# Performance work log

Hardware: AMD Instinct MI355X
Metric: run time of the kernel (lower is better)

The kernel has to match this reference:

```python
import jax, jax.numpy as jnp
import numpy as np

B, S, D_IN, D_OUT = 8, 2048, 1024, 1024


def setup_inputs() -> dict:
    key = jax.random.key(0)
    ks = jax.random.split(key, 9)
    sc = 1.0 / np.sqrt(D_IN)
    return {
        "in_k": jax.random.normal(ks[0], (B, S, D_IN), jnp.float32),
        "in_q": jax.random.normal(ks[1], (B, S, D_IN), jnp.float32),
        "in_v": jax.random.normal(ks[2], (B, S, D_IN), jnp.float32),
        "Wk": jax.random.normal(ks[3], (D_IN, D_OUT), jnp.float32) * sc,
        "bk": jax.random.normal(ks[4], (D_OUT,), jnp.float32) * sc,
        "Wq": jax.random.normal(ks[5], (D_IN, D_OUT), jnp.float32) * sc,
        "bq": jax.random.normal(ks[6], (D_OUT,), jnp.float32) * sc,
        "Wv": jax.random.normal(ks[7], (D_IN, D_OUT), jnp.float32) * sc,
        "bv": jax.random.normal(ks[8], (D_OUT,), jnp.float32) * sc,
    }


def reference(in_k, in_q, in_v, Wk, bk, Wq, bq, Wv, bv):
    k = in_k @ Wk + bk  # [B,S,D]
    q = in_q @ Wq + bq
    v = in_v @ Wv + bv
    scale = 1.0 / jnp.sqrt(jnp.asarray(D_OUT, q.dtype))
    scores = jnp.einsum("bqd,bkd->bqk", q, k) * scale  # [B,S,S]
    attn = jax.nn.softmax(scores, axis=-1)
    return jnp.einsum("bqk,bkd->bqd", attn, v)
```

## Files before the change

kernel.cpp:

```cpp
#include <hip/hip_runtime.h>
#include <hip/hip_bf16.h>
#include <stdint.h>

typedef __bf16 bf16x8 __attribute__((ext_vector_type(8)));
typedef float  f32x4  __attribute__((ext_vector_type(4)));
typedef uint16_t u16x8 __attribute__((ext_vector_type(8)));

__device__ __forceinline__ uint16_t f32_to_bf16(float f) {
    union { float f; uint32_t u; } v; v.f = f;
    uint32_t u = v.u;
    uint32_t r = (u + 0x7FFFu + ((u >> 16) & 1u)) >> 16;
    return (uint16_t)r;
}

__device__ __forceinline__ void gld16(const void* g, void* l) {
    __builtin_amdgcn_global_load_lds(
        (const __attribute__((address_space(1))) void*)g,
        (__attribute__((address_space(3))) void*)l,
        16, 0, 0);
}

#define MFMA16 __builtin_amdgcn_mfma_f32_16x16x32_bf16
#define SBAR   __builtin_amdgcn_s_barrier
#define SCHED0() __builtin_amdgcn_sched_barrier(0)
#define PRIO   __builtin_amdgcn_s_setprio
#define VMCNT4() asm volatile("s_waitcnt vmcnt(4)" ::: "memory")
#define VMCNT0() asm volatile("s_waitcnt vmcnt(0)" ::: "memory")

__global__ __launch_bounds__(256) void cast3_kernel(
    const float* __restrict__ i0, const float* __restrict__ i1,
    const float* __restrict__ i2, uint16_t* __restrict__ o0,
    uint16_t* __restrict__ o1, uint16_t* __restrict__ o2) {
    const float* in = (blockIdx.z == 0) ? i0 : (blockIdx.z == 1) ? i1 : i2;
    uint16_t* out = (blockIdx.z == 0) ? o0 : (blockIdx.z == 1) ? o1 : o2;
    size_t i = ((size_t)blockIdx.x * 256 + threadIdx.x) * 8;
    float4 a = *(const float4*)(in + i);
    float4 b = *(const float4*)(in + i + 4);
    u16x8 o;
    o[0] = f32_to_bf16(a.x); o[1] = f32_to_bf16(a.y);
    o[2] = f32_to_bf16(a.z); o[3] = f32_to_bf16(a.w);
    o[4] = f32_to_bf16(b.x); o[5] = f32_to_bf16(b.y);
    o[6] = f32_to_bf16(b.z); o[7] = f32_to_bf16(b.w);
    *(u16x8*)(out + i) = o;
}

__global__ __launch_bounds__(256) void wtrans_kernel(
    const float* __restrict__ W0, const float* __restrict__ W1,
    const float* __restrict__ W2, uint16_t* __restrict__ Wt0) {
    const float* W = (blockIdx.z == 0) ? W0 : (blockIdx.z == 1) ? W1 : W2;
    uint16_t* Wt = Wt0 + (size_t)blockIdx.z * 1024 * 1024;
    __shared__ float tile[64][65];
    const int n0 = blockIdx.x * 64, k0 = blockIdx.y * 64;
    const int tx = threadIdx.x & 63, ty0 = threadIdx.x >> 6;
#pragma unroll
    for (int r = 0; r < 16; ++r) {
        int ty = ty0 + r * 4;
        tile[ty][tx] = W[(size_t)(k0 + ty) * 1024 + n0 + tx];
    }
    __syncthreads();
#pragma unroll
    for (int r = 0; r < 16; ++r) {
        int ty = ty0 + r * 4;
        Wt[(size_t)(n0 + ty) * 1024 + k0 + tx] = f32_to_bf16(tile[tx][ty]);
    }
}

__device__ __forceinline__ void stageA64(const uint16_t* __restrict__ G, int ldg,
                                         int k0, int rowbase, uint16_t* ldsT, int tid) {
    const int l = tid >> 3;
    const int ch = tid & 7;
    const int c = ((ch ^ (l & 7)) << 3);
    gld16(G + (size_t)(rowbase + l) * ldg + k0 + c,
          ldsT + (size_t)(rowbase + l) * 64 + ch * 8);
}

__device__ __forceinline__ void stageB64(const uint16_t* __restrict__ G, int ldg,
                                         int k0, int h, int j, uint16_t* ldsT, int tid) {
    const int lloc = j * 64 + (tid >> 3);
    const int ch = tid & 7;
    const int grow = (lloc & 31) + ((lloc >> 5) << 6) + (h << 5);
    const int c = ((ch ^ (lloc & 7)) << 3);
    gld16(G + (size_t)grow * ldg + k0 + c,
          ldsT + (size_t)(h * 128 + lloc) * 64 + ch * 8);
}

__device__ __forceinline__ void gemm_core(const uint16_t* __restrict__ A, int lda,
                                          const uint16_t* __restrict__ B, int ldb,
                                          int K, f32x4 (&acc)[8][4]) {
    __shared__ __align__(16) uint16_t As[2][16384];
    __shared__ __align__(16) uint16_t Bs[2][16384];
    const int tid  = threadIdx.x;
    const int lane = tid & 63;
    const int wave = tid >> 6;
    const int wr = wave >> 2, wcn = wave & 3;
    const int mrow = lane & 15, q = lane >> 4;
    const int sx = mrow & 7;
    const int c0 = ((q ^ sx) << 3);
    const int c1 = (((4 + q) ^ sx) << 3);
    const int abase = (wr * 128 + mrow) * 64;
    const int bb    = (wcn * 32 + mrow) * 64;

    const int NT = K >> 6;
    stageA64(A, lda, 0, 0,   As[0], tid);
    stageA64(A, lda, 0, 128, As[0], tid);
    SCHED0();
    stageB64(B, ldb, 0, 0, 0, Bs[0], tid);
    stageB64(B, ldb, 0, 0, 1, Bs[0], tid);
    SCHED0();
    stageB64(B, ldb, 0, 1, 0, Bs[0], tid);
    stageB64(B, ldb, 0, 1, 1, Bs[0], tid);
    SCHED0();
    stageA64(A, lda, 0, 64,  As[0], tid);
    stageA64(A, lda, 0, 192, As[0], tid);
    SCHED0();

    bf16x8 af[4][2], bA[2][2], bB[2][2];
    for (int t = 0; t < NT; ++t) {
        const int cur = t & 1;
        const uint16_t* as = As[cur];
        const uint16_t* bs = Bs[cur];
        uint16_t* An = As[cur ^ 1];
        uint16_t* Bn = Bs[cur ^ 1];
        const int kn = (t + 1 < NT) ? ((t + 1) << 6) : 0;

        VMCNT4();
        SBAR(); SCHED0();
        stageA64(A, lda, kn, 0,   An, tid);
        stageA64(A, lda, kn, 128, An, tid);
#pragma unroll
        for (int m = 0; m < 4; ++m) {
            af[m][0] = *(const bf16x8*)&as[abase + m * 1024 + c0];
            af[m][1] = *(const bf16x8*)&as[abase + m * 1024 + c1];
        }
#pragma unroll
        for (int n = 0; n < 2; ++n) {
            bA[n][0] = *(const bf16x8*)&bs[bb + n * 1024 + c0];
            bA[n][1] = *(const bf16x8*)&bs[bb + n * 1024 + c1];
        }
        SBAR(); SCHED0();
        PRIO(1);
#pragma unroll
        for (int m = 0; m < 4; ++m)
#pragma unroll
            for (int n = 0; n < 2; ++n) {
                acc[m][n] = MFMA16(af[m][0], bA[n][0], acc[m][n], 0, 0, 0);
                acc[m][n] = MFMA16(af[m][1], bA[n][1], acc[m][n], 0, 0, 0);
            }
        PRIO(0);

        VMCNT4();
        SBAR(); SCHED0();
        stageB64(B, ldb, kn, 0, 0, Bn, tid);
        stageB64(B, ldb, kn, 0, 1, Bn, tid);
#pragma unroll
        for (int n = 0; n < 2; ++n) {
            bB[n][0] = *(const bf16x8*)&bs[bb + 8192 + n * 1024 + c0];
            bB[n][1] = *(const bf16x8*)&bs[bb + 8192 + n * 1024 + c1];
        }
        SBAR(); SCHED0();
        PRIO(1);
#pragma unroll
        for (int m = 0; m < 4; ++m)
#pragma unroll
            for (int n = 0; n < 2; ++n) {
                acc[m][n + 2] = MFMA16(af[m][0], bB[n][0], acc[m][n + 2], 0, 0, 0);
                acc[m][n + 2] = MFMA16(af[m][1], bB[n][1], acc[m][n + 2], 0, 0, 0);
            }
        PRIO(0);

        VMCNT4();
        SBAR(); SCHED0();
        stageB64(B, ldb, kn, 1, 0, Bn, tid);
        stageB64(B, ldb, kn, 1, 1, Bn, tid);
#pragma unroll
        for (int m = 0; m < 4; ++m) {
            af[m][0] = *(const bf16x8*)&as[abase + (m + 4) * 1024 + c0];
            af[m][1] = *(const bf16x8*)&as[abase + (m + 4) * 1024 + c1];
        }
        SBAR(); SCHED0();
        PRIO(1);
#pragma unroll
        for (int m = 0; m < 4; ++m)
#pragma unroll
            for (int n = 0; n < 2; ++n) {
                acc[m + 4][n] = MFMA16(af[m][0], bA[n][0], acc[m + 4][n], 0, 0, 0);
                acc[m + 4][n] = MFMA16(af[m][1], bA[n][1], acc[m + 4][n], 0, 0, 0);
            }
        PRIO(0);

        SBAR(); SCHED0();
        stageA64(A, lda, kn, 64,  An, tid);
        stageA64(A, lda, kn, 192, An, tid);
        SBAR(); SCHED0();
        PRIO(1);
#pragma unroll
        for (int m = 0; m < 4; ++m)
#pragma unroll
            for (int n = 0; n < 2; ++n) {
                acc[m + 4][n + 2] = MFMA16(af[m][0], bB[n][0], acc[m + 4][n + 2], 0, 0, 0);
                acc[m + 4][n + 2] = MFMA16(af[m][1], bB[n][1], acc[m + 4][n + 2], 0, 0, 0);
            }
        PRIO(0);
    }
    VMCNT0();
}

__global__ __launch_bounds__(512, 2) void proj256_kernel(
    const uint16_t* __restrict__ Ab, const uint16_t* __restrict__ Bb,
    uint16_t* __restrict__ Cb, uint16_t* __restrict__ Vt,
    const float* __restrict__ b0, const float* __restrict__ b1,
    const float* __restrict__ b2) {
    const int bid = blockIdx.x;
    const int lg = (bid & 7) * 96 + (bid >> 3);
    const int pidx = lg >> 8;
    const int t = lg & 255;
    const int band = t >> 4;
    const int Mt = band * 4 + (t & 3);
    const int Nt = (t >> 2) & 3;
    const int row0 = Mt * 256, col0 = Nt * 256;

    const uint16_t* A = Ab + (size_t)pidx * 16777216 + (size_t)row0 * 1024;
    const uint16_t* B = Bb + (size_t)pidx * 1048576 + (size_t)col0 * 1024;
    const float* bias = (pidx == 0) ? b0 : (pidx == 1) ? b1 : b2;

    f32x4 acc[8][4];
#pragma unroll
    for (int i = 0; i < 8; ++i)
#pragma unroll
        for (int j = 0; j < 4; ++j) acc[i][j] = 0.0f;

    gemm_core(A, 1024, B, 1024, 1024, acc);

    const int tid = threadIdx.x, lane = tid & 63, wave = tid >> 6;
    const int wr = wave >> 2, wcn = wave & 3;
    const int mrow = lane & 15, quad = lane >> 4;
    float bv_[4];
#pragma unroll
    for (int n = 0; n < 4; ++n) bv_[n] = bias[col0 + wcn * 64 + n * 16 + mrow];

    if (pidx < 2) {
        uint16_t* C = Cb + (size_t)pidx * 16777216;
#pragma unroll
        for (int m = 0; m < 8; ++m)
#pragma unroll
            for (int n = 0; n < 4; ++n)
#pragma unroll
                for (int r = 0; r < 4; ++r) {
                    int row = row0 + wr * 128 + m * 16 + quad * 4 + r;
                    int col = col0 + wcn * 64 + n * 16 + mrow;
                    C[(size_t)row * 1024 + col] = f32_to_bf16(acc[m][n][r] + bv_[n]);
                }
    } else {
#pragma unroll
        for (int m = 0; m < 8; ++m)
#pragma unroll
            for (int n = 0; n < 4; ++n)
#pragma unroll
                for (int r = 0; r < 4; ++r) {
                    int row = row0 + wr * 128 + m * 16 + quad * 4 + r;
                    int col = col0 + wcn * 64 + n * 16 + mrow;
                    Vt[((size_t)(row >> 11) * 1024 + col) * 2048 + (row & 2047)] =
                        f32_to_bf16(acc[m][n][r] + bv_[n]);
                }
    }
}

template <int EPI>
__global__ __launch_bounds__(512, 2) void att256_kernel(
    const uint16_t* __restrict__ Abase, int lda, long long sAz,
    const uint16_t* __restrict__ Bbase, int ldb, long long sBz,
    void* __restrict__ Cv, int ldc, long long sCz,
    int K, float alpha, float* __restrict__ sums, int NtN, int chunk) {
    const int bid = blockIdx.x;
    const int lg = (bid & 7) * chunk + (bid >> 3);
    const int z = lg / chunk;
    const int t = lg % chunk;
    const int r2 = t & (2 * NtN - 1);
    const int band = t / (2 * NtN);
    const int Mt = band * 2 + (r2 & 1);
    const int Nt = r2 >> 1;
    const int row0 = Mt * 256, col0 = Nt * 256;

    const uint16_t* A = Abase + (size_t)z * sAz + (size_t)row0 * lda;
    const uint16_t* B = Bbase + (size_t)z * sBz + (size_t)col0 * ldb;

    f32x4 acc[8][4];
#pragma unroll
    for (int i = 0; i < 8; ++i)
#pragma unroll
        for (int j = 0; j < 4; ++j) acc[i][j] = 0.0f;

    gemm_core(A, lda, B, ldb, K, acc);

    const int tid = threadIdx.x, lane = tid & 63, wave = tid >> 6;
    const int wr = wave >> 2, wcn = wave & 3;
    const int mrow = lane & 15, quad = lane >> 4;

    if (EPI == 1) {
        uint16_t* C = (uint16_t*)Cv + (size_t)z * sCz;
#pragma unroll
        for (int m = 0; m < 8; ++m)
#pragma unroll
            for (int r = 0; r < 4; ++r) {
                int row = row0 + wr * 128 + m * 16 + quad * 4 + r;
                float s = 0.0f;
#pragma unroll
                for (int n = 0; n < 4; ++n) {
                    int col = col0 + wcn * 64 + n * 16 + mrow;
                    float e = __expf(acc[m][n][r] * alpha);
                    C[(size_t)row * ldc + col] = f32_to_bf16(e);
                    s += e;
                }
                s += __shfl_xor(s, 1, 64);
                s += __shfl_xor(s, 2, 64);
                s += __shfl_xor(s, 4, 64);
                s += __shfl_xor(s, 8, 64);
                if (mrow == 0) atomicAdd(&sums[(size_t)z * 2048 + row], s);
            }
    } else {
        float* C = (float*)Cv + (size_t)z * sCz;
#pragma unroll
        for (int m = 0; m < 8; ++m)
#pragma unroll
            for (int r = 0; r < 4; ++r) {
                int row = row0 + wr * 128 + m * 16 + quad * 4 + r;
                float inv = 1.0f / sums[(size_t)z * 2048 + row];
#pragma unroll
                for (int n = 0; n < 4; ++n) {
                    int col = col0 + wcn * 64 + n * 16 + mrow;
                    C[(size_t)row * ldc + col] = acc[m][n][r] * inv;
                }
            }
    }
}

extern "C" void kernel_launch(void* const* d_in, const int* in_sizes, int n_in,
                              void* d_out, int out_size, void* d_ws, size_t ws_size,
                              hipStream_t stream) {
    const float* in_k = (const float*)d_in[0];
    const float* in_q = (const float*)d_in[1];
    const float* in_v = (const float*)d_in[2];
    const float* Wk = (const float*)d_in[3];
    const float* bk = (const float*)d_in[4];
    const float* Wq = (const float*)d_in[5];
    const float* bq = (const float*)d_in[6];
    const float* Wv = (const float*)d_in[7];
    const float* bv = (const float*)d_in[8];
    float* out = (float*)d_out;

    char* w = (char*)d_ws;
    uint16_t* Xq  = (uint16_t*)(w + 0);
    uint16_t* Xk  = (uint16_t*)(w + 33554432);
    uint16_t* Xv  = (uint16_t*)(w + 67108864);
    uint16_t* Qb  = (uint16_t*)(w + 100663296);
    uint16_t* Kb  = (uint16_t*)(w + 134217728);
    uint16_t* Vt  = (uint16_t*)(w + 167772160);
    uint16_t* Wqt = (uint16_t*)(w + 201326592);
    uint16_t* Sc  = Xq;
    float*    sums = (float*)Xv;

    wtrans_kernel<<<dim3(16, 16, 3), 256, 0, stream>>>(Wq, Wk, Wv, Wqt);
    cast3_kernel<<<dim3(8192, 1, 3), 256, 0, stream>>>(in_q, in_k, in_v, Xq, Xk, Xv);

    proj256_kernel<<<768, 512, 0, stream>>>(Xq, Wqt, Qb, Vt, bq, bk, bv);

    hipMemsetAsync(sums, 0, 8 * 2048 * sizeof(float), stream);

    att256_kernel<1><<<512, 512, 0, stream>>>(
        Qb, 1024, 2048LL * 1024, Kb, 1024, 2048LL * 1024,
        Sc, 2048, 2048LL * 2048, 1024, 0.03125f, sums, 8, 64);

    att256_kernel<2><<<256, 512, 0, stream>>>(
        Sc, 2048, 2048LL * 2048, Vt, 2048, 1024LL * 2048,
        out, 1024, 2048LL * 1024, 2048, 1.0f, sums, 4, 32);
}
```

Before: 517.6 us.

## Software-pipeline LDS fragment reads one phase ahead of MFMA in projection GEMM

Restructures the projection GEMM main loop into a two-iteration unrolled 8-phase schedule. Each phase's LDS fragment reads for the next MFMA block are issued before the current MFMA block, using ping-pong register sets (Xa/Ya, Xb/Yb). Partial lgkmcnt and vmcnt waits let loads overlap compute instead of stalling on each read. This adds register pressure from the duplicated fragments and KEEP asm hacks to keep the dead prefetches alive. It also assumes NT is even and that the finer-grained waits are correct.

Measured after the change: 609.2 us. 1.18x slower.

```diff
diff --git a/kernel.cpp b/kernel.cpp
--- a/kernel.cpp
+++ b/kernel.cpp
@@ -24,8 +24,11 @@
 #define SBAR   __builtin_amdgcn_s_barrier
 #define SCHED0() __builtin_amdgcn_sched_barrier(0)
 #define PRIO   __builtin_amdgcn_s_setprio
-#define VMCNT4() asm volatile("s_waitcnt vmcnt(4)" ::: "memory")
+#define VMC2()   asm volatile("s_waitcnt vmcnt(2)" ::: "memory")
 #define VMCNT0() asm volatile("s_waitcnt vmcnt(0)" ::: "memory")
+#define LGKM4()  asm volatile("s_waitcnt lgkmcnt(4)" ::: "memory")
+#define LGKM8()  asm volatile("s_waitcnt lgkmcnt(8)" ::: "memory")
+#define KEEP(x)  asm volatile("" :: "v"(*(const float*)&(x)))
 
 __global__ __launch_bounds__(256) void cast3_kernel(
     const float* __restrict__ i0, const float* __restrict__ i1,
@@ -84,6 +87,37 @@
           ldsT + (size_t)(h * 128 + lloc) * 64 + ch * 8);
 }
 
+__device__ __forceinline__ void rdA(bf16x8 (&dst)[4][2], const uint16_t* s,
+                                    int abase, int mb, int c0, int c1) {
+#pragma unroll
+    for (int m = 0; m < 4; ++m) {
+        dst[m][0] = *(const bf16x8*)&s[abase + (mb + m) * 1024 + c0];
+        dst[m][1] = *(const bf16x8*)&s[abase + (mb + m) * 1024 + c1];
+    }
+}
+
+__device__ __forceinline__ void rdB(bf16x8 (&dst)[2][2], const uint16_t* s,
+                                    int bb, int h, int c0, int c1) {
+#pragma unroll
+    for (int n = 0; n < 2; ++n) {
+        dst[n][0] = *(const bf16x8*)&s[bb + h * 8192 + n * 1024 + c0];
+        dst[n][1] = *(const bf16x8*)&s[bb + h * 8192 + n * 1024 + c1];
+    }
+}
+
+__device__ __forceinline__ void mm8(f32x4 (&acc)[8][4], int mb, int nh,
+                                    const bf16x8 (&a)[4][2], const bf16x8 (&b)[2][2]) {
+#pragma unroll
+    for (int m = 0; m < 4; ++m)
+#pragma unroll
+        for (int n = 0; n < 2; ++n) {
+            acc[mb + m][nh * 2 + n] =
+                MFMA16(a[m][0], b[n][0], acc[mb + m][nh * 2 + n], 0, 0, 0);
+            acc[mb + m][nh * 2 + n] =
+                MFMA16(a[m][1], b[n][1], acc[mb + m][nh * 2 + n], 0, 0, 0);
+        }
+}
+
 __device__ __forceinline__ void gemm_core(const uint16_t* __restrict__ A, int lda,
                                           const uint16_t* __restrict__ B, int ldb,
                                           int K, f32x4 (&acc)[8][4]) {
@@ -100,109 +134,69 @@
     const int abase = (wr * 128 + mrow) * 64;
     const int bb    = (wcn * 32 + mrow) * 64;
 
+    uint16_t* As0 = As[0]; uint16_t* As1 = As[1];
+    uint16_t* Bs0 = Bs[0]; uint16_t* Bs1 = Bs[1];
+
+    bf16x8 Xa[4][2], Ya[4][2], Xb[2][2], Yb[2][2];
+
+    stageA64(A, lda, 0, 0,   As0, tid); stageA64(A, lda, 0, 128, As0, tid);
+    stageB64(B, ldb, 0, 0, 0, Bs0, tid); stageB64(B, ldb, 0, 0, 1, Bs0, tid);
+    stageB64(B, ldb, 0, 1, 0, Bs0, tid); stageB64(B, ldb, 0, 1, 1, Bs0, tid);
+    stageA64(A, lda, 0, 64,  As0, tid); stageA64(A, lda, 0, 192, As0, tid);
+    VMCNT0();
+    __syncthreads();
+    rdA(Xa, As0, abase, 0, c0, c1);
+    rdB(Xb, Bs0, bb, 0, c0, c1);
+
     const int NT = K >> 6;
-    stageA64(A, lda, 0, 0,   As[0], tid);
-    stageA64(A, lda, 0, 128, As[0], tid);
-    SCHED0();
-    stageB64(B, ldb, 0, 0, 0, Bs[0], tid);
-    stageB64(B, ldb, 0, 0, 1, Bs[0], tid);
-    SCHED0();
-    stageB64(B, ldb, 0, 1, 0, Bs[0], tid);
-    stageB64(B, ldb, 0, 1, 1, Bs[0], tid);
-    SCHED0();
-    stageA64(A, lda, 0, 64,  As[0], tid);
-    stageA64(A, lda, 0, 192, As[0], tid);
-    SCHED0();
-
-    bf16x8 af[4][2], bA[2][2], bB[2][2];
-    for (int t = 0; t < NT; ++t) {
-        const int cur = t & 1;
-        const uint16_t* as = As[cur];
-        const uint16_t* bs = Bs[cur];
-        uint16_t* An = As[cur ^ 1];
-        uint16_t* Bn = Bs[cur ^ 1];
-        const int kn = (t + 1 < NT) ? ((t + 1) << 6) : 0;
-
-        VMCNT4();
-        SBAR(); SCHED0();
-        stageA64(A, lda, kn, 0,   An, tid);
-        stageA64(A, lda, kn, 128, An, tid);
-#pragma unroll
-        for (int m = 0; m < 4; ++m) {
-            af[m][0] = *(const bf16x8*)&as[abase + m * 1024 + c0];
-            af[m][1] = *(const bf16x8*)&as[abase + m * 1024 + c1];
-        }
-#pragma unroll
-        for (int n = 0; n < 2; ++n) {
-            bA[n][0] = *(const bf16x8*)&bs[bb + n * 1024 + c0];
-            bA[n][1] = *(const bf16x8*)&bs[bb + n * 1024 + c1];
-        }
-        SBAR(); SCHED0();
-        PRIO(1);
-#pragma unroll
-        for (int m = 0; m < 4; ++m)
-#pragma unroll
-            for (int n = 0; n < 2; ++n) {
-                acc[m][n] = MFMA16(af[m][0], bA[n][0], acc[m][n], 0, 0, 0);
-                acc[m][n] = MFMA16(af[m][1], bA[n][1], acc[m][n], 0, 0, 0);
-            }
-        PRIO(0);
-
-        VMCNT4();
-        SBAR(); SCHED0();
-        stageB64(B, ldb, kn, 0, 0, Bn, tid);
-        stageB64(B, ldb, kn, 0, 1, Bn, tid);
-#pragma unroll
-        for (int n = 0; n < 2; ++n) {
-            bB[n][0] = *(const bf16x8*)&bs[bb + 8192 + n * 1024 + c0];
-            bB[n][1] = *(const bf16x8*)&bs[bb + 8192 + n * 1024 + c1];
-        }
-        SBAR(); SCHED0();
-        PRIO(1);
-#pragma unroll
-        for (int m = 0; m < 4; ++m)
-#pragma unroll
-            for (int n = 0; n < 2; ++n) {
-                acc[m][n + 2] = MFMA16(af[m][0], bB[n][0], acc[m][n + 2], 0, 0, 0);
-                acc[m][n + 2] = MFMA16(af[m][1], bB[n][1], acc[m][n + 2], 0, 0, 0);
-            }
-        PRIO(0);
-
-        VMCNT4();
-        SBAR(); SCHED0();
-        stageB64(B, ldb, kn, 1, 0, Bn, tid);
-        stageB64(B, ldb, kn, 1, 1, Bn, tid);
-#pragma unroll
-        for (int m = 0; m < 4; ++m) {
-            af[m][0] = *(const bf16x8*)&as[abase + (m + 4) * 1024 + c0];
-            af[m][1] = *(const bf16x8*)&as[abase + (m + 4) * 1024 + c1];
-        }
-        SBAR(); SCHED0();
-        PRIO(1);
-#pragma unroll
-        for (int m = 0; m < 4; ++m)
-#pragma unroll
-            for (int n = 0; n < 2; ++n) {
-                acc[m + 4][n] = MFMA16(af[m][0], bA[n][0], acc[m + 4][n], 0, 0, 0);
-                acc[m + 4][n] = MFMA16(af[m][1], bA[n][1], acc[m + 4][n], 0, 0, 0);
-            }
-        PRIO(0);
-
-        SBAR(); SCHED0();
-        stageA64(A, lda, kn, 64,  An, tid);
-        stageA64(A, lda, kn, 192, An, tid);
-        SBAR(); SCHED0();
-        PRIO(1);
-#pragma unroll
-        for (int m = 0; m < 4; ++m)
-#pragma unroll
-            for (int n = 0; n < 2; ++n) {
-                acc[m + 4][n + 2] = MFMA16(af[m][0], bB[n][0], acc[m + 4][n + 2], 0, 0, 0);
-                acc[m + 4][n + 2] = MFMA16(af[m][1], bB[n][1], acc[m + 4][n + 2], 0, 0, 0);
-            }
-        PRIO(0);
+    for (int it = 0; it < NT; it += 2) {
+        const int k1 = (it + 1) << 6;
+        const int k2 = (it + 2 < NT) ? ((it + 2) << 6) : 0;
+
+        rdB(Yb, Bs0, bb, 1, c0, c1);
+        stageA64(A, lda, k1, 0, As1, tid); stageA64(A, lda, k1, 128, As1, tid);
+        VMC2(); SBAR(); LGKM4(); SCHED0();
+        PRIO(1); mm8(acc, 0, 0, Xa, Xb); PRIO(0); SBAR(); SCHED0();
+
+        rdA(Ya, As0, abase, 4, c0, c1);
+        stageB64(B, ldb, k1, 0, 0, Bs1, tid); stageB64(B, ldb, k1, 0, 1, Bs1, tid);
+        VMC2(); SBAR(); LGKM8(); SCHED0();
+        PRIO(1); mm8(acc, 0, 1, Xa, Yb); PRIO(0); SBAR(); SCHED0();
+
+        rdA(Xa, As1, abase, 0, c0, c1);
+        stageB64(B, ldb, k1, 1, 0, Bs1, tid); stageB64(B, ldb, k1, 1, 1, Bs1, tid);
+        VMC2(); SBAR(); LGKM8(); SCHED0();
+        PRIO(1); mm8(acc, 4, 1, Ya, Yb); PRIO(0); SBAR(); SCHED0();
+
+        rdB(Yb, Bs1, bb, 0, c0, c1);
+        stageA64(A, lda, k1, 64, As1, tid); stageA64(A, lda, k1, 192, As1, tid);
+        VMC2(); SBAR(); LGKM4(); SCHED0();
+        PRIO(1); mm8(acc, 4, 0, Ya, Xb); PRIO(0); SBAR(); SCHED0();
+
+        rdB(Xb, Bs1, bb, 1, c0, c1);
+        stageA64(A, lda, k2, 0, As0, tid); stageA64(A, lda, k2, 128, As0, tid);
+        VMC2(); SBAR(); LGKM4(); SCHED0();
+        PRIO(1); mm8(acc, 0, 0, Xa, Yb); PRIO(0); SBAR(); SCHED0();
+
+        rdA(Ya, As1, abase, 4, c0, c1);
+        stageB64(B, ldb, k2, 0, 0, Bs0, tid); stageB64(B, ldb, k2, 0, 1, Bs0, tid);
+        VMC2(); SBAR(); LGKM8(); SCHED0();
+        PRIO(1); mm8(acc, 0, 1, Xa, Xb); PRIO(0); SBAR(); SCHED0();
+
+        rdA(Xa, As0, abase, 0, c0, c1);
+        stageB64(B, ldb, k2, 1, 0, Bs0, tid); stageB64(B, ldb, k2, 1, 1, Bs0, tid);
+        VMC2(); SBAR(); LGKM8(); SCHED0();
+        PRIO(1); mm8(acc, 4, 1, Ya, Xb); PRIO(0); SBAR(); SCHED0();
+
+        rdB(Xb, Bs0, bb, 0, c0, c1);
+        stageA64(A, lda, k2, 64, As0, tid); stageA64(A, lda, k2, 192, As0, tid);
+        VMC2(); SBAR(); LGKM4(); SCHED0();
+        PRIO(1); mm8(acc, 4, 0, Ya, Yb); PRIO(0); SBAR(); SCHED0();
     }
     VMCNT0();
+    KEEP(Xa[0][0]); KEEP(Xa[0][1]); KEEP(Xa[1][0]); KEEP(Xa[1][1]);
+    KEEP(Xa[2][0]); KEEP(Xa[2][1]); KEEP(Xa[3][0]); KEEP(Xa[3][1]);
+    KEEP(Xb[0][0]); KEEP(Xb[0][1]); KEEP(Xb[1][0]); KEEP(Xb[1][1]);
 }
 
 __global__ __launch_bounds__(512, 2) void proj256_kernel(
```
